# Optimization experiments

Measured on AMD Instinct MI355X. Metric: run time of the kernel, lower is better.

The kernel has to match this reference:

```python
import jax, jax.numpy as jnp
import numpy as np

NUM_HEADS = 4
EPS = 1e-5

def _proj(x, W, b):
    # 1x1x1 Conv3d == channel-wise linear: x [B,C,H,W,D], W [Cout,Cin], b [Cout]
    return jnp.einsum('oc,bchwd->bohwd', W, x) + b[None, :, None, None, None]

def setup_inputs() -> dict:
    key = jax.random.key(0)
    ks = jax.random.split(key, 12)
    B, C, H, W, D = 2, 128, 16, 16, 16
    s = 1.0 / np.sqrt(C)
    inp = {
        'query_features': jax.random.normal(ks[0], (B, C, H, W, D), jnp.float32),
        'key_value_features': jax.random.normal(ks[1], (B, C, H, W, D), jnp.float32),
        'Wq': jax.random.normal(ks[2], (C, C), jnp.float32) * s,
        'bq': jax.random.normal(ks[3], (C,), jnp.float32) * 0.01,
        'Wk': jax.random.normal(ks[4], (C, C), jnp.float32) * s,
        'bk': jax.random.normal(ks[5], (C,), jnp.float32) * 0.01,
        'Wv': jax.random.normal(ks[6], (C, C), jnp.float32) * s,
        'bv': jax.random.normal(ks[7], (C,), jnp.float32) * 0.01,
        'Wo': jax.random.normal(ks[8], (C, C), jnp.float32) * s,
        'bo': jax.random.normal(ks[9], (C,), jnp.float32) * 0.01,
    }
    return inp

def reference(query_features, key_value_features, Wq, bq, Wk, bk, Wv, bv, Wo, bo):
    B, C, H, W, D = query_features.shape
    hd = C // NUM_HEADS  # head_dim
    N = H * W * D
    Q = _proj(query_features, Wq, bq).reshape(B, NUM_HEADS, hd, N)
    K = _proj(key_value_features, Wk, bk).reshape(B, NUM_HEADS, hd, N)
    V = _proj(key_value_features, Wv, bv).reshape(B, NUM_HEADS, hd, N)
    scale = hd ** -0.5
    attn = jnp.einsum('bhdn,bhdm->bhnm', Q, K) * scale  # [B,h,N,N]
    attn = jax.nn.softmax(attn, axis=-1)
    out = jnp.einsum('bhnm,bhdm->bhdn', attn, V).reshape(B, C, H, W, D)
    out = _proj(out, Wo, bo)
    res = query_features + out
    # InstanceNorm3d (affine=False): normalize over spatial dims per (B,C)
    mu = jnp.mean(res, axis=(2, 3, 4), keepdims=True)
    var = jnp.var(res, axis=(2, 3, 4), keepdims=True)
    return (res - mu) * jax.lax.rsqrt(var + EPS)
```

## Files before the change

kernel.cpp:

```cpp
#include <hip/hip_runtime.h>
#include <hip/hip_bf16.h>

typedef unsigned short u16;
typedef unsigned int u32;
typedef __bf16 bf16_t;
typedef bf16_t bf16x8 __attribute__((ext_vector_type(8)));
typedef float f32x4 __attribute__((ext_vector_type(4)));

#define NTOT 4096
#define CCH 128
#define QSCL 0.25503486703f

__device__ __forceinline__ float bf2f(u16 x) {
    return __uint_as_float(((u32)x) << 16);
}
__device__ __forceinline__ u32 pkbf(float a, float b) {
    __hip_bfloat162 h = __float22bfloat162_rn(make_float2(a, b));
    u32 r; __builtin_memcpy(&r, &h, 4); return r;
}
__device__ __forceinline__ u16 f2bf(float a) {
    return (u16)(pkbf(a, a) & 0xffffu);
}

__global__ __launch_bounds__(256, 4) void proj_kernel(
    const float* __restrict__ xq, const float* __restrict__ xkv,
    const float* __restrict__ Wq, const float* __restrict__ bq,
    const float* __restrict__ Wk, const float* __restrict__ bk_,
    const float* __restrict__ Wv, const float* __restrict__ bv_,
    u16* __restrict__ Qt, u16* __restrict__ Kt, u16* __restrict__ Vn)
{
    const int nt = blockIdx.x, p = blockIdx.y, b = blockIdx.z;
    const float* X    = (p == 0) ? xq : xkv;
    const float* Wf   = (p == 0) ? Wq : (p == 1) ? Wk : Wv;
    const float* bias = (p == 0) ? bq : (p == 1) ? bk_ : bv_;
    const float s = (p == 0) ? QSCL : 1.0f;
    const int n0 = nt * 64;
    const int tid = threadIdx.x;

    __shared__ u16 Xt[64 * 128];
    __shared__ u16 Wl[128 * 136];

    #pragma unroll
    for (int k = 0; k < 4; ++k) {
        int n = tid & 63;
        int c = (tid >> 6) + k * 4;
        float f[8];
        #pragma unroll
        for (int j = 0; j < 8; ++j)
            f[j] = X[((size_t)(b * CCH) + 8 * c + j) * NTOT + n0 + n];
        uint4 vv = {pkbf(f[0], f[1]), pkbf(f[2], f[3]), pkbf(f[4], f[5]), pkbf(f[6], f[7])};
        *(uint4*)(Xt + n * 128 + ((c ^ (n & 7)) * 8)) = vv;
    }
    #pragma unroll
    for (int k = 0; k < 8; ++k) {
        int id = tid + k * 256;
        int row = id >> 4;
        int off = (id & 15) * 8;
        const float* wsrc = Wf + row * 128 + off;
        float4 wa = *(const float4*)(wsrc);
        float4 wc = *(const float4*)(wsrc + 4);
        uint4 vv = {pkbf(wa.x * s, wa.y * s), pkbf(wa.z * s, wa.w * s),
                    pkbf(wc.x * s, wc.y * s), pkbf(wc.z * s, wc.w * s)};
        *(uint4*)(Wl + row * 136 + off) = vv;
    }
    __syncthreads();

    const int wave = tid >> 6, lane = tid & 63;
    const int quad = lane >> 4, l16 = lane & 15;
    f32x4 acc[8];
    #pragma unroll
    for (int cf = 0; cf < 8; ++cf) acc[cf] = (f32x4){0.f, 0.f, 0.f, 0.f};

    #pragma unroll
    for (int kk = 0; kk < 4; ++kk) {
        bf16x8 bx = *(const bf16x8*)(Xt + (wave * 16 + l16) * 128 +
                                     (((kk * 4 + quad) ^ (l16 & 7)) * 8));
        #pragma unroll
        for (int cf = 0; cf < 8; ++cf) {
            bf16x8 aw = *(const bf16x8*)(Wl + (cf * 16 + l16) * 136 + kk * 32 + quad * 8);
            acc[cf] = __builtin_amdgcn_mfma_f32_16x16x32_bf16(aw, bx, acc[cf], 0, 0, 0);
        }
    }

    const int n = n0 + wave * 16 + l16;
    #pragma unroll
    for (int cf = 0; cf < 8; ++cf) {
        float4 b4 = *(const float4*)(bias + cf * 16 + quad * 4);
        float v0 = acc[cf][0] + b4.x * s;
        float v1 = acc[cf][1] + b4.y * s;
        float v2 = acc[cf][2] + b4.z * s;
        float v3 = acc[cf][3] + b4.w * s;
        if (p < 2) {
            const int h = cf >> 1;
            const int d0 = (cf & 1) * 16 + quad * 4;
            u16* dst = (p == 0 ? Qt : Kt) + ((size_t)(b * 4 + h) * NTOT + n) * 32 + d0;
            uint2 vv = {pkbf(v0, v1), pkbf(v2, v3)};
            *(uint2*)dst = vv;
        } else {
            int c = cf * 16 + quad * 4;
            u16* dst = Vn + (size_t)(b * CCH + c) * NTOT + n;
            dst[0 * NTOT] = f2bf(v0); dst[1 * NTOT] = f2bf(v1);
            dst[2 * NTOT] = f2bf(v2); dst[3 * NTOT] = f2bf(v3);
        }
    }
}

__global__ __launch_bounds__(256, 2) void flash_attn_kernel(
    const u16* __restrict__ Qt, const u16* __restrict__ Kt,
    const u16* __restrict__ Vn, u16* __restrict__ pO, float* __restrict__ pL)
{
    const int bh = blockIdx.z, kc = blockIdx.y;
    const int wave = threadIdx.x >> 6, lane = threadIdx.x & 63;
    const int q = lane >> 4, l16 = lane & 15;
    const int q0w = blockIdx.x * 256 + wave * 64;

    const u16* Qbh = Qt + (size_t)bh * NTOT * 32;
    const u16* Kbh = Kt + (size_t)bh * NTOT * 32;
    const u16* Vg  = Vn + ((size_t)((bh >> 2) * CCH + (bh & 3) * 32)) * NTOT;

    __shared__ u16 Kb[2][2048];
    __shared__ u16 Vb[2][2048];

    const int kbase = kc * 1024;

    bf16x8 bq[4];
    #pragma unroll
    for (int g = 0; g < 4; ++g)
        bq[g] = *(const bf16x8*)(Qbh + (size_t)(q0w + g * 16 + l16) * 32 + q * 8);

    const size_t ksrc = (size_t)(wave * 16 + l16) * 32 + q * 8;
    const size_t vsrc = (size_t)((wave & 1) * 16 + l16) * NTOT + (wave >> 1) * 32 + q * 8;
    const int k_dst = wave * 512 + lane * 8;
    const int v_dst = wave * 512 + (q & 1) * 256 + l16 * 8 + (q >> 1) * 4;

    uint4 kreg = *(const uint4*)(Kbh + (size_t)kbase * 32 + ksrc);
    uint4 vreg = *(const uint4*)(Vg + vsrc + kbase);
    *(uint4*)(&Kb[0][k_dst]) = kreg;
    {
        uint2 va = {vreg.x, vreg.y}, vb2 = {vreg.z, vreg.w};
        *(uint2*)(&Vb[0][v_dst])       = va;
        *(uint2*)(&Vb[0][v_dst + 128]) = vb2;
    }
    __syncthreads();

    f32x4 o[4][2];
    #pragma unroll
    for (int g = 0; g < 4; ++g) {
        o[g][0] = (f32x4){0,0,0,0};
        o[g][1] = (f32x4){0,0,0,0};
    }
    const f32x4 zero = {0,0,0,0};
    float lp[4] = {0.f, 0.f, 0.f, 0.f};

    for (int it = 0; it < 16; ++it) {
        const int cur = it & 1;
        if (it < 15) {
            const int m1 = kbase + (it + 1) * 64;
            kreg = *(const uint4*)(Kbh + (size_t)m1 * 32 + ksrc);
            vreg = *(const uint4*)(Vg + vsrc + m1);
        }
        f32x4 s[4][4];
        #pragma unroll
        for (int t = 0; t < 4; ++t) {
            bf16x8 ak = *(const bf16x8*)(&Kb[cur][t * 512 + lane * 8]);
            #pragma unroll
            for (int g = 0; g < 4; ++g)
                s[g][t] = __builtin_amdgcn_mfma_f32_16x16x32_bf16(ak, bq[g], zero, 0, 0, 0);
        }
        bf16x8 av00 = *(const bf16x8*)(&Vb[cur][0 * 512 + lane * 8]);
        bf16x8 av01 = *(const bf16x8*)(&Vb[cur][1 * 512 + lane * 8]);
        bf16x8 av10 = *(const bf16x8*)(&Vb[cur][2 * 512 + lane * 8]);
        bf16x8 av11 = *(const bf16x8*)(&Vb[cur][3 * 512 + lane * 8]);
        #pragma unroll
        for (int g = 0; g < 4; ++g) {
            float e[4][4];
            #pragma unroll
            for (int t = 0; t < 4; ++t) {
                e[t][0] = __builtin_amdgcn_exp2f(s[g][t][0]);
                e[t][1] = __builtin_amdgcn_exp2f(s[g][t][1]);
                e[t][2] = __builtin_amdgcn_exp2f(s[g][t][2]);
                e[t][3] = __builtin_amdgcn_exp2f(s[g][t][3]);
                lp[g] += (e[t][0] + e[t][1]) + (e[t][2] + e[t][3]);
            }
            uint4 u0 = {pkbf(e[0][0], e[0][1]), pkbf(e[0][2], e[0][3]),
                        pkbf(e[1][0], e[1][1]), pkbf(e[1][2], e[1][3])};
            uint4 u1 = {pkbf(e[2][0], e[2][1]), pkbf(e[2][2], e[2][3]),
                        pkbf(e[3][0], e[3][1]), pkbf(e[3][2], e[3][3])};
            bf16x8 pb0, pb1;
            __builtin_memcpy(&pb0, &u0, 16);
            __builtin_memcpy(&pb1, &u1, 16);
            o[g][0] = __builtin_amdgcn_mfma_f32_16x16x32_bf16(av00, pb0, o[g][0], 0, 0, 0);
            o[g][1] = __builtin_amdgcn_mfma_f32_16x16x32_bf16(av01, pb0, o[g][1], 0, 0, 0);
            o[g][0] = __builtin_amdgcn_mfma_f32_16x16x32_bf16(av10, pb1, o[g][0], 0, 0, 0);
            o[g][1] = __builtin_amdgcn_mfma_f32_16x16x32_bf16(av11, pb1, o[g][1], 0, 0, 0);
        }
        if (it < 15) {
            const int nb = (it + 1) & 1;
            *(uint4*)(&Kb[nb][k_dst]) = kreg;
            uint2 va = {vreg.x, vreg.y}, vb2 = {vreg.z, vreg.w};
            *(uint2*)(&Vb[nb][v_dst])       = va;
            *(uint2*)(&Vb[nb][v_dst + 128]) = vb2;
        }
        __syncthreads();
    }

    #pragma unroll
    for (int g = 0; g < 4; ++g) {
        lp[g] += __shfl_xor(lp[g], 16);
        lp[g] += __shfl_xor(lp[g], 32);
        const size_t ob = ((size_t)(kc * 8 + bh) * NTOT + q0w + g * 16 + l16) * 32 + q * 4;
        uint2 w0 = {pkbf(o[g][0][0], o[g][0][1]), pkbf(o[g][0][2], o[g][0][3])};
        uint2 w1 = {pkbf(o[g][1][0], o[g][1][1]), pkbf(o[g][1][2], o[g][1][3])};
        *(uint2*)(pO + ob)      = w0;
        *(uint2*)(pO + ob + 16) = w1;
        if (q == 0)
            pL[(size_t)(kc * 8 + bh) * NTOT + q0w + g * 16 + l16] = lp[g];
    }
}

__global__ __launch_bounds__(256, 4) void outproj_kernel(
    const float* __restrict__ xq,
    const u16* __restrict__ pO, const float* __restrict__ pL,
    const float* __restrict__ Wo, const float* __restrict__ bo,
    float* __restrict__ res, float* __restrict__ partS, float* __restrict__ partQ)
{
    const int nt = blockIdx.x, ct = blockIdx.y, b = blockIdx.z;
    const int n0 = nt * 64;
    const int tid = threadIdx.x;

    __shared__ u16 Xt[64 * 128];
    __shared__ u16 Wl[64 * 136];

    #pragma unroll
    for (int k = 0; k < 4; ++k) {
        int cid = tid + k * 256;
        int n = cid >> 4;
        int ch = cid & 15;
        int bh = b * 4 + (ch >> 2);
        int d0 = (ch & 3) * 8;
        float l = 0.f;
        float v[8];
        #pragma unroll
        for (int j = 0; j < 8; ++j) v[j] = 0.f;
        #pragma unroll
        for (int kcc = 0; kcc < 4; ++kcc) {
            const size_t nrow = (size_t)(kcc * 8 + bh) * NTOT + n0 + n;
            l += pL[nrow];
            uint4 u = *(const uint4*)(pO + nrow * 32 + d0);
            const u32 uu[4] = {u.x, u.y, u.z, u.w};
            #pragma unroll
            for (int j = 0; j < 4; ++j) {
                v[2 * j]     += bf2f((u16)(uu[j] & 0xffffu));
                v[2 * j + 1] += bf2f((u16)(uu[j] >> 16));
            }
        }
        const float inv = 1.0f / l;
        uint4 vv = {pkbf(v[0] * inv, v[1] * inv), pkbf(v[2] * inv, v[3] * inv),
                    pkbf(v[4] * inv, v[5] * inv), pkbf(v[6] * inv, v[7] * inv)};
        *(uint4*)(Xt + n * 128 + ((ch ^ (n & 7)) * 8)) = vv;
    }
    #pragma unroll
    for (int k = 0; k < 4; ++k) {
        int id = tid + k * 256;
        int row = id >> 4;
        int off = (id & 15) * 8;
        const float* wsrc = Wo + (size_t)(ct * 64 + row) * 128 + off;
        float4 wa = *(const float4*)(wsrc);
        float4 wc = *(const float4*)(wsrc + 4);
        uint4 vv = {pkbf(wa.x, wa.y), pkbf(wa.z, wa.w),
                    pkbf(wc.x, wc.y), pkbf(wc.z, wc.w)};
        *(uint4*)(Wl + row * 136 + off) = vv;
    }
    __syncthreads();

    const int wave = tid >> 6, lane = tid & 63;
    const int quad = lane >> 4, l16 = lane & 15;
    f32x4 acc[4];
    #pragma unroll
    for (int cf = 0; cf < 4; ++cf) acc[cf] = (f32x4){0.f, 0.f, 0.f, 0.f};

    #pragma unroll
    for (int kk = 0; kk < 4; ++kk) {
        bf16x8 bx = *(const bf16x8*)(Xt + (wave * 16 + l16) * 128 +
                                     (((kk * 4 + quad) ^ (l16 & 7)) * 8));
        #pragma unroll
        for (int cf = 0; cf < 4; ++cf) {
            bf16x8 aw = *(const bf16x8*)(Wl + (cf * 16 + l16) * 136 + kk * 32 + quad * 8);
            acc[cf] = __builtin_amdgcn_mfma_f32_16x16x32_bf16(aw, bx, acc[cf], 0, 0, 0);
        }
    }

    const int n = n0 + wave * 16 + l16;
    const int tile = nt * 4 + wave;
    #pragma unroll
    for (int cf = 0; cf < 4; ++cf) {
        float4 b4 = *(const float4*)(bo + ct * 64 + cf * 16 + quad * 4);
        const float bb[4] = {b4.x, b4.y, b4.z, b4.w};
        float sv[4], qv[4];
        #pragma unroll
        for (int r = 0; r < 4; ++r) {
            int c = ct * 64 + cf * 16 + quad * 4 + r;
            float v = acc[cf][r] + bb[r] + xq[(size_t)(b * CCH + c) * NTOT + n];
            res[(size_t)(b * CCH + c) * NTOT + n] = v;
            sv[r] = v;
            qv[r] = v * v;
        }
        #pragma unroll
        for (int off = 1; off < 16; off <<= 1) {
            #pragma unroll
            for (int r = 0; r < 4; ++r) {
                sv[r] += __shfl_xor(sv[r], off);
                qv[r] += __shfl_xor(qv[r], off);
            }
        }
        if (l16 == 0) {
            #pragma unroll
            for (int r = 0; r < 4; ++r) {
                int c = ct * 64 + cf * 16 + quad * 4 + r;
                partS[(size_t)(b * CCH + c) * 256 + tile] = sv[r];
                partQ[(size_t)(b * CCH + c) * 256 + tile] = qv[r];
            }
        }
    }
}

__global__ __launch_bounds__(256) void norm_kernel(
    const float* __restrict__ res, const float* __restrict__ partS,
    const float* __restrict__ partQ, float* __restrict__ out)
{
    const int c = blockIdx.x, b = blockIdx.y;
    const int tid = threadIdx.x;
    const size_t row = (size_t)(b * CCH + c);
    __shared__ float rs[4], rq[4];
    float s = partS[row * 256 + tid];
    float q = partQ[row * 256 + tid];
    #pragma unroll
    for (int off = 1; off < 64; off <<= 1) {
        s += __shfl_xor(s, off);
        q += __shfl_xor(q, off);
    }
    const int wv = tid >> 6, ln = tid & 63;
    if (ln == 0) { rs[wv] = s; rq[wv] = q; }
    __syncthreads();
    float ts = rs[0] + rs[1] + rs[2] + rs[3];
    float tq = rq[0] + rq[1] + rq[2] + rq[3];
    float mu  = ts * (1.0f / 4096.0f);
    float var = tq * (1.0f / 4096.0f) - mu * mu;
    float inv = rsqrtf(var + 1e-5f);
    const size_t base = row * NTOT;
    #pragma unroll
    for (int j = 0; j < 4; ++j) {
        int n = tid * 4 + j * 1024;
        float4 v = *(const float4*)(res + base + n);
        float4 o;
        o.x = (v.x - mu) * inv; o.y = (v.y - mu) * inv;
        o.z = (v.z - mu) * inv; o.w = (v.w - mu) * inv;
        *(float4*)(out + base + n) = o;
    }
}

extern "C" void kernel_launch(void* const* d_in, const int* in_sizes, int n_in,
                              void* d_out, int out_size, void* d_ws, size_t ws_size,
                              hipStream_t stream)
{
    const float* xq  = (const float*)d_in[0];
    const float* xkv = (const float*)d_in[1];
    const float* Wq  = (const float*)d_in[2];
    const float* bq  = (const float*)d_in[3];
    const float* Wk  = (const float*)d_in[4];
    const float* bk  = (const float*)d_in[5];
    const float* Wv  = (const float*)d_in[6];
    const float* bv  = (const float*)d_in[7];
    const float* Wo  = (const float*)d_in[8];
    const float* bo  = (const float*)d_in[9];
    float* out = (float*)d_out;

    char* ws = (char*)d_ws;
    const size_t MB = (size_t)1 << 20;
    u16* Qt = (u16*)(ws + 0 * MB);
    u16* Kt = (u16*)(ws + 2 * MB);
    u16* Vn = (u16*)(ws + 4 * MB);
    u16* pO = (u16*)(ws + 6 * MB);
    float* pL = (float*)(ws + 14 * MB);
    float* res   = (float*)(ws + 16 * MB);
    float* partS = (float*)(ws + 20 * MB);
    float* partQ = (float*)(ws + 20 * MB + 262144);

    proj_kernel<<<dim3(64, 3, 2), 256, 0, stream>>>(xq, xkv, Wq, bq, Wk, bk, Wv, bv, Qt, Kt, Vn);
    flash_attn_kernel<<<dim3(16, 4, 8), 256, 0, stream>>>(Qt, Kt, Vn, pO, pL);
    outproj_kernel<<<dim3(64, 2, 2), 256, 0, stream>>>(xq, pO, pL, Wo, bo, res, partS, partQ);
    norm_kernel<<<dim3(128, 2), 256, 0, stream>>>(res, partS, partQ, out);
}
```

Measured before the change: 120.1 us.

## Load K/V fragments directly from global into registers, drop LDS staging

The flash attention kernel no longer stages K and V tiles through double-buffered shared memory with block-wide barriers. Each wave now loads its own MFMA operand fragments straight from global memory (L2/cache) into registers, prefetching the next tile one iteration ahead. This removes the LDS round trip and the __syncthreads per iteration. In exchange, each of the four waves fetches the same K/V data redundantly, so global/L2 traffic rises fourfold and register pressure goes up. V is loaded with split 8-byte accesses.

```diff
diff --git a/kernel.cpp b/kernel.cpp
--- a/kernel.cpp
+++ b/kernel.cpp
@@ -20,6 +20,12 @@
 }
 __device__ __forceinline__ u16 f2bf(float a) {
     return (u16)(pkbf(a, a) & 0xffffu);
+}
+__device__ __forceinline__ bf16x8 ldv(const u16* p) {
+    uint2 lo = *(const uint2*)(p);
+    uint2 hi = *(const uint2*)(p + 16);
+    uint4 u = {lo.x, lo.y, hi.x, hi.y};
+    bf16x8 r; __builtin_memcpy(&r, &u, 16); return r;
 }
 
 __global__ __launch_bounds__(256, 4) void proj_kernel(
@@ -118,9 +124,6 @@
     const u16* Kbh = Kt + (size_t)bh * NTOT * 32;
     const u16* Vg  = Vn + ((size_t)((bh >> 2) * CCH + (bh & 3) * 32)) * NTOT;
 
-    __shared__ u16 Kb[2][2048];
-    __shared__ u16 Vb[2][2048];
-
     const int kbase = kc * 1024;
 
     bf16x8 bq[4];
@@ -128,20 +131,9 @@
     for (int g = 0; g < 4; ++g)
         bq[g] = *(const bf16x8*)(Qbh + (size_t)(q0w + g * 16 + l16) * 32 + q * 8);
 
-    const size_t ksrc = (size_t)(wave * 16 + l16) * 32 + q * 8;
-    const size_t vsrc = (size_t)((wave & 1) * 16 + l16) * NTOT + (wave >> 1) * 32 + q * 8;
-    const int k_dst = wave * 512 + lane * 8;
-    const int v_dst = wave * 512 + (q & 1) * 256 + l16 * 8 + (q >> 1) * 4;
-
-    uint4 kreg = *(const uint4*)(Kbh + (size_t)kbase * 32 + ksrc);
-    uint4 vreg = *(const uint4*)(Vg + vsrc + kbase);
-    *(uint4*)(&Kb[0][k_dst]) = kreg;
-    {
-        uint2 va = {vreg.x, vreg.y}, vb2 = {vreg.z, vreg.w};
-        *(uint2*)(&Vb[0][v_dst])       = va;
-        *(uint2*)(&Vb[0][v_dst + 128]) = vb2;
-    }
-    __syncthreads();
+    const u16* kp  = Kbh + (size_t)(kbase + l16) * 32 + q * 8;
+    const u16* vp0 = Vg + (size_t)l16 * NTOT + kbase + q * 4;
+    const u16* vp1 = vp0 + (size_t)16 * NTOT;
 
     f32x4 o[4][2];
     #pragma unroll
@@ -152,25 +144,32 @@
     const f32x4 zero = {0,0,0,0};
     float lp[4] = {0.f, 0.f, 0.f, 0.f};
 
+    bf16x8 ak[4], av[4];
+    #pragma unroll
+    for (int t = 0; t < 4; ++t)
+        ak[t] = *(const bf16x8*)(kp + (size_t)(t * 16) * 32);
+    #pragma unroll
+    for (int r = 0; r < 4; ++r)
+        av[r] = ldv(((r & 1) ? vp1 : vp0) + (r >> 1) * 32);
+
     for (int it = 0; it < 16; ++it) {
-        const int cur = it & 1;
+        bf16x8 nak[4], nav[4];
         if (it < 15) {
-            const int m1 = kbase + (it + 1) * 64;
-            kreg = *(const uint4*)(Kbh + (size_t)m1 * 32 + ksrc);
-            vreg = *(const uint4*)(Vg + vsrc + m1);
+            const int m1 = (it + 1) * 64;
+            #pragma unroll
+            for (int t = 0; t < 4; ++t)
+                nak[t] = *(const bf16x8*)(kp + (size_t)(m1 + t * 16) * 32);
+            #pragma unroll
+            for (int r = 0; r < 4; ++r)
+                nav[r] = ldv(((r & 1) ? vp1 : vp0) + m1 + (r >> 1) * 32);
         }
         f32x4 s[4][4];
         #pragma unroll
         for (int t = 0; t < 4; ++t) {
-            bf16x8 ak = *(const bf16x8*)(&Kb[cur][t * 512 + lane * 8]);
             #pragma unroll
             for (int g = 0; g < 4; ++g)
-                s[g][t] = __builtin_amdgcn_mfma_f32_16x16x32_bf16(ak, bq[g], zero, 0, 0, 0);
-        }
-        bf16x8 av00 = *(const bf16x8*)(&Vb[cur][0 * 512 + lane * 8]);
-        bf16x8 av01 = *(const bf16x8*)(&Vb[cur][1 * 512 + lane * 8]);
-        bf16x8 av10 = *(const bf16x8*)(&Vb[cur][2 * 512 + lane * 8]);
-        bf16x8 av11 = *(const bf16x8*)(&Vb[cur][3 * 512 + lane * 8]);
+                s[g][t] = __builtin_amdgcn_mfma_f32_16x16x32_bf16(ak[t], bq[g], zero, 0, 0, 0);
+        }
         #pragma unroll
         for (int g = 0; g < 4; ++g) {
             float e[4][4];
@@ -189,19 +188,17 @@
             bf16x8 pb0, pb1;
             __builtin_memcpy(&pb0, &u0, 16);
             __builtin_memcpy(&pb1, &u1, 16);
-            o[g][0] = __builtin_amdgcn_mfma_f32_16x16x32_bf16(av00, pb0, o[g][0], 0, 0, 0);
-            o[g][1] = __builtin_amdgcn_mfma_f32_16x16x32_bf16(av01, pb0, o[g][1], 0, 0, 0);
-            o[g][0] = __builtin_amdgcn_mfma_f32_16x16x32_bf16(av10, pb1, o[g][0], 0, 0, 0);
-            o[g][1] = __builtin_amdgcn_mfma_f32_16x16x32_bf16(av11, pb1, o[g][1], 0, 0, 0);
+            o[g][0] = __builtin_amdgcn_mfma_f32_16x16x32_bf16(av[0], pb0, o[g][0], 0, 0, 0);
+            o[g][1] = __builtin_amdgcn_mfma_f32_16x16x32_bf16(av[1], pb0, o[g][1], 0, 0, 0);
+            o[g][0] = __builtin_amdgcn_mfma_f32_16x16x32_bf16(av[2], pb1, o[g][0], 0, 0, 0);
+            o[g][1] = __builtin_amdgcn_mfma_f32_16x16x32_bf16(av[3], pb1, o[g][1], 0, 0, 0);
         }
         if (it < 15) {
-            const int nb = (it + 1) & 1;
-            *(uint4*)(&Kb[nb][k_dst]) = kreg;
-            uint2 va = {vreg.x, vreg.y}, vb2 = {vreg.z, vreg.w};
-            *(uint2*)(&Vb[nb][v_dst])       = va;
-            *(uint2*)(&Vb[nb][v_dst + 128]) = vb2;
-        }
-        __syncthreads();
+            #pragma unroll
+            for (int t = 0; t < 4; ++t) ak[t] = nak[t];
+            #pragma unroll
+            for (int r = 0; r < 4; ++r) av[r] = nav[r];
+        }
     }
 
     #pragma unroll
```

New measurement: 131.7 us. +9.7%, slower.
